# Kernel optimization log

Hardware: AMD Instinct MI355X
Metric: run time of the kernel (lower is better)

The kernel has to match this reference:

```python
import jax, jax.numpy as jnp
import numpy as np

D_MODEL = 1024
N_HEADS = 16
HEAD_DIM = D_MODEL // N_HEADS


def setup_inputs() -> dict:
    key = jax.random.key(0)
    ks = jax.random.split(key, 5)
    x = jax.random.normal(ks[0], (4, 2048, D_MODEL), dtype=jnp.float32)
    # qkv Linear: weight [3*d_model, d_model], bias [3*d_model]
    w_qkv = jax.random.normal(ks[1], (3 * D_MODEL, D_MODEL), dtype=jnp.float32) / np.sqrt(D_MODEL)
    b_qkv = jnp.zeros((3 * D_MODEL,), dtype=jnp.float32)
    w_out = jax.random.normal(ks[2], (D_MODEL, D_MODEL), dtype=jnp.float32) / np.sqrt(D_MODEL)
    b_out = jnp.zeros((D_MODEL,), dtype=jnp.float32)
    return {"x": x, "w_qkv": w_qkv, "b_qkv": b_qkv, "w_out": w_out, "b_out": b_out}


def reference(x, w_qkv, b_qkv, w_out, b_out):
    B, T, C = x.shape
    H, Dh = N_HEADS, HEAD_DIM
    qkv = x @ w_qkv.T + b_qkv                      # [B,T,3C]
    qkv = qkv.reshape(B, T, 3, H, Dh)
    q = jnp.transpose(qkv[:, :, 0], (0, 2, 1, 3))  # [B,H,T,Dh]
    k = jnp.transpose(qkv[:, :, 1], (0, 2, 1, 3))
    v = jnpp_transpose = jnp.transpose(qkv[:, :, 2], (0, 2, 1, 3))
    scale = 1.0 / np.sqrt(Dh).astype(np.float32)
    att = jnp.einsum('bhqd,bhkd->bhqk', q, k) * scale
    causal = jnp.tril(jnp.ones((T, T), dtype=bool))
    att = jnp.where(causal[None, None], att, -jnp.inf)
    att = jax.nn.softmax(att, axis=-1)
    head_out = jnp.einsum('bhqk,bhkd->bhqd', att, v)  # [B,H,T,Dh]
    out = jnp.transpose(head_out, (0, 2, 1, 3)).reshape(B, T, C)
    return out @ w_out.T + b_out
```

## Files before the change

kernel.cpp:

```cpp
#include <hip/hip_runtime.h>
#include <hip/hip_bf16.h>


#define D_MODEL 1024
#define N_HEADS 16
#define HEAD_DIM 64
#define SEQ 2048
#define BATCH 4

typedef __attribute__((ext_vector_type(8))) short bf16x8;
typedef __attribute__((ext_vector_type(4))) float f32x4;
typedef unsigned int uint;

__device__ __forceinline__ short f2bf(float f) {
    union { float f; uint i; } c; c.f = f;
    uint x = c.i;
    x += 0x7fffu + ((x >> 16) & 1u);
    return (short)(x >> 16);
}
__device__ __forceinline__ uint pack2(float a, float b) {
    return (uint)(unsigned short)f2bf(a) | ((uint)(unsigned short)f2bf(b) << 16);
}
__device__ __forceinline__ uint asu(float f) { union { float f; uint i; } c; c.f = f; return c.i; }
__device__ __forceinline__ uint packtr(float lo, float hi) {
    return (asu(lo) >> 16) | (asu(hi) & 0xffff0000u);
}

__device__ __forceinline__ void glds16(const void* g, void* l) {
    __builtin_amdgcn_global_load_lds(
        (const __attribute__((address_space(1))) uint*)g,
        (__attribute__((address_space(3))) uint*)l, 16, 0, 0);
}

__global__ __launch_bounds__(256) void cvt3_bf16(const float* __restrict__ s0,
                                                 const float* __restrict__ s1,
                                                 const float* __restrict__ s2,
                                                 short* __restrict__ dst,
                                                 int n0, int n01) {
    int i = blockIdx.x * 256 + threadIdx.x;
    const float* src;
    int off;
    if (i < n0)       { src = s0; off = i; }
    else if (i < n01) { src = s1; off = i - n0; }
    else              { src = s2; off = i - n01; }
    float4 f = *(const float4*)(src + (size_t)off * 4);
    uint2 o; o.x = pack2(f.x, f.y); o.y = pack2(f.z, f.w);
    *(uint2*)(dst + (size_t)i * 4) = o;
}

template <int MODE>
__global__ __launch_bounds__(256, 2) void gemm_bt(
    const short* __restrict__ A, const short* __restrict__ B,
    const float* __restrict__ bias, float* __restrict__ Cp,
    int M, int N, int K,
    short* __restrict__ qp, short* __restrict__ kp, short* __restrict__ vp)
{
    __shared__ short As[128][32];
    __shared__ short Bs[128][32];
    const int tid = threadIdx.x;
    const int wave = tid >> 6, lane = tid & 63;
    const int quad = lane >> 4, l16 = lane & 15;
    const int wm = (wave >> 1) * 64, wn = (wave & 1) * 64;
    const int rowBase = blockIdx.y * 128;
    const int colBase = blockIdx.x * 128;

    const short* gA = A + (size_t)(rowBase + wave * 32 + (lane >> 2)) * K + (lane & 3) * 8;
    const short* gB = B + (size_t)(colBase + wave * 32 + (lane >> 2)) * K + (lane & 3) * 8;
    void* lA0 = &As[wave * 32][0];
    void* lA1 = &As[wave * 32 + 16][0];
    void* lB0 = &Bs[wave * 32][0];
    void* lB1 = &Bs[wave * 32 + 16][0];

    f32x4 acc[4][4] = {};

    for (int k0 = 0; k0 < K; k0 += 32) {
        __syncthreads();
        glds16(gA + k0, lA0);
        glds16(gA + (size_t)16 * K + k0, lA1);
        glds16(gB + k0, lB0);
        glds16(gB + (size_t)16 * K + k0, lB1);
        __syncthreads();
        bf16x8 af[4], bfr[4];
#pragma unroll
        for (int i = 0; i < 4; ++i)
            af[i] = *(const bf16x8*)&As[wm + i * 16 + l16][quad * 8];
#pragma unroll
        for (int j = 0; j < 4; ++j)
            bfr[j] = *(const bf16x8*)&Bs[wn + j * 16 + l16][quad * 8];
#pragma unroll
        for (int i = 0; i < 4; ++i)
#pragma unroll
            for (int j = 0; j < 4; ++j)
                acc[i][j] = __builtin_amdgcn_mfma_f32_16x16x32_bf16(af[i], bfr[j], acc[i][j], 0, 0, 0);
    }

#pragma unroll
    for (int i = 0; i < 4; ++i) {
#pragma unroll
        for (int j = 0; j < 4; ++j) {
#pragma unroll
            for (int r = 0; r < 4; ++r) {
                int row = rowBase + wm + i * 16 + quad * 4 + r;
                int col = colBase + wn + j * 16 + l16;
                float v = acc[i][j][r] + bias[col];
                if (MODE == 0) {
                    Cp[(size_t)row * N + col] = v;
                } else {
                    int which = col >> 10;
                    int h = (col >> 6) & 15;
                    int d = col & 63;
                    int b = row >> 11;
                    int t = row & 2047;
                    short* dst = (which == 0) ? qp : (which == 1) ? kp : vp;
                    dst[((((size_t)b * N_HEADS + h) * SEQ) + t) * HEAD_DIM + d] = f2bf(v);
                }
            }
        }
    }
}

__global__ __launch_bounds__(256, 2) void attn_fwd(
    const short* __restrict__ Q, const short* __restrict__ K,
    const short* __restrict__ V, short* __restrict__ O)
{
    __shared__ short Ks[64][72];
    __shared__ short Vt[64][72];
    __shared__ short Ps[128][72];
    const int tid = threadIdx.x;
    const int wave = tid >> 6, lane = tid & 63;
    const int quad = lane >> 4, l16 = lane & 15;
    const int bh = blockIdx.x;
    const int b = bh >> 4, h = bh & 15;
    const short* Qh = Q + (size_t)bh * SEQ * HEAD_DIM;
    const short* Kh = K + (size_t)bh * SEQ * HEAD_DIM;
    const short* Vh = V + (size_t)bh * SEQ * HEAD_DIM;

    const float C1 = 0.125f * 1.44269504f;
    const float C2 = 14.4269504f;

    bf16x8 onesf;
#pragma unroll
    for (int e = 0; e < 8; ++e) onesf[e] = (short)0x3F80;

    const int kr = tid >> 2, kc = (tid & 3) * 16;
    const int vk = (tid & 31) * 2, vd = (tid >> 5) * 8;

    for (int pass = 0; pass < 2; ++pass) {
        const int qt = pass == 0 ? (15 - (int)blockIdx.y) : (int)blockIdx.y;
        const int qbase = qt * 128;

        bf16x8 qf[2][2];
#pragma unroll
        for (int m = 0; m < 2; ++m)
#pragma unroll
            for (int st = 0; st < 2; ++st)
                qf[m][st] = *(const bf16x8*)(Qh + (size_t)(qbase + wave * 32 + m * 16 + l16) * HEAD_DIM + st * 32 + quad * 8);

        f32x4 o[2][4] = {};
        f32x4 osum[2] = {};

        const int subw = qbase + wave * 32;
        const int subS = __builtin_amdgcn_readfirstlane(subw);

        const int ntiles = 2 * qt + 2;
        int4 kv0 = *(const int4*)(Kh + (size_t)kr * HEAD_DIM + kc);
        int4 kv1 = *(const int4*)(Kh + (size_t)kr * HEAD_DIM + kc + 8);
        int4 vv0 = *(const int4*)(Vh + (size_t)vk * HEAD_DIM + vd);
        int4 vv1 = *(const int4*)(Vh + (size_t)(vk + 1) * HEAD_DIM + vd);

        for (int j = 0; j < ntiles; ++j) {
            const int kb = j * 64;
            __syncthreads();
            *(int4*)&Ks[kr][kc] = kv0;
            *(int4*)&Ks[kr][kc + 8] = kv1;
            {
                const uint* pa = (const uint*)&vv0;
                const uint* pb = (const uint*)&vv1;
#pragma unroll
                for (int e = 0; e < 4; ++e) {
                    uint lo = __builtin_amdgcn_perm(pb[e], pa[e], 0x05040100u);
                    uint hi = __builtin_amdgcn_perm(pb[e], pa[e], 0x07060302u);
                    *(uint*)&Vt[vd + 2 * e][vk] = lo;
                    *(uint*)&Vt[vd + 2 * e + 1][vk] = hi;
                }
            }
            __syncthreads();

            {
                const int kbn = (j + 1 < ntiles) ? kb + 64 : kb;
                kv0 = *(const int4*)(Kh + (size_t)(kbn + kr) * HEAD_DIM + kc);
                kv1 = *(const int4*)(Kh + (size_t)(kbn + kr) * HEAD_DIM + kc + 8);
                vv0 = *(const int4*)(Vh + (size_t)(kbn + vk) * HEAD_DIM + vd);
                vv1 = *(const int4*)(Vh + (size_t)(kbn + vk + 1) * HEAD_DIM + vd);
            }

            if (kb > subS + 31) continue;

            f32x4 s[2][4];
#pragma unroll
            for (int kt = 0; kt < 4; ++kt) {
                bf16x8 kf0 = *(const bf16x8*)&Ks[kt * 16 + l16][quad * 8];
                bf16x8 kf1 = *(const bf16x8*)&Ks[kt * 16 + l16][32 + quad * 8];
#pragma unroll
                for (int m = 0; m < 2; ++m) {
                    f32x4 t = {0.f, 0.f, 0.f, 0.f};
                    t = __builtin_amdgcn_mfma_f32_16x16x32_bf16(kf0, qf[m][0], t, 0, 0, 0);
                    t = __builtin_amdgcn_mfma_f32_16x16x32_bf16(kf1, qf[m][1], t, 0, 0, 0);
                    s[m][kt] = t;
                }
            }
#pragma unroll
            for (int m = 0; m < 2; ++m) {
                const int sub = subS + m * 16;
                const int qrow = sub + l16;
                const int prow = wave * 32 + m * 16 + l16;
#pragma unroll
                for (int kt = 0; kt < 4; ++kt) {
                    const int kbkt = kb + kt * 16;
                    uint2 u;
                    if (kbkt > sub + 15) {
                        u.x = 0u; u.y = 0u;
                    } else if (kbkt + 15 <= sub) {
                        float p[4];
#pragma unroll
                        for (int r = 0; r < 4; ++r)
                            p[r] = __builtin_exp2f(__builtin_fmaf(s[m][kt][r], C1, -C2));
                        u.x = packtr(p[0], p[1]); u.y = packtr(p[2], p[3]);
                    } else {
                        float p[4];
#pragma unroll
                        for (int r = 0; r < 4; ++r) {
                            float a = __builtin_fmaf(s[m][kt][r], C1, -C2);
                            if (kbkt + quad * 4 + r > qrow) a = -1e30f;
                            p[r] = __builtin_exp2f(a);
                        }
                        u.x = packtr(p[0], p[1]); u.y = packtr(p[2], p[3]);
                    }
                    *(uint2*)&Ps[prow][kt * 16 + quad * 4] = u;
                }
            }
#pragma unroll
            for (int st = 0; st < 2; ++st) {
                bf16x8 pf0 = *(const bf16x8*)&Ps[wave * 32 + l16][st * 32 + quad * 8];
                bf16x8 pf1 = *(const bf16x8*)&Ps[wave * 32 + 16 + l16][st * 32 + quad * 8];
                osum[0] = __builtin_amdgcn_mfma_f32_16x16x32_bf16(pf0, onesf, osum[0], 0, 0, 0);
                osum[1] = __builtin_amdgcn_mfma_f32_16x16x32_bf16(pf1, onesf, osum[1], 0, 0, 0);
#pragma unroll
                for (int dt = 0; dt < 4; ++dt) {
                    bf16x8 vf = *(const bf16x8*)&Vt[dt * 16 + l16][st * 32 + quad * 8];
                    o[0][dt] = __builtin_amdgcn_mfma_f32_16x16x32_bf16(pf0, vf, o[0][dt], 0, 0, 0);
                    o[1][dt] = __builtin_amdgcn_mfma_f32_16x16x32_bf16(pf1, vf, o[1][dt], 0, 0, 0);
                }
            }
        }

#pragma unroll
        for (int m = 0; m < 2; ++m) {
#pragma unroll
            for (int r = 0; r < 4; ++r) {
                float inv = 1.f / osum[m][r];
                int t = qbase + wave * 32 + m * 16 + quad * 4 + r;
                size_t base = ((size_t)b * SEQ + t) * D_MODEL + h * HEAD_DIM;
#pragma unroll
                for (int dt = 0; dt < 4; ++dt)
                    O[base + dt * 16 + l16] = f2bf(o[m][dt][r] * inv);
            }
        }
    }
}

extern "C" void kernel_launch(void* const* d_in, const int* in_sizes, int n_in,
                              void* d_out, int out_size, void* d_ws, size_t ws_size,
                              hipStream_t stream)
{
    const float* x     = (const float*)d_in[0];
    const float* w_qkv = (const float*)d_in[1];
    const float* b_qkv = (const float*)d_in[2];
    const float* w_out = (const float*)d_in[3];
    const float* b_out = (const float*)d_in[4];
    float* out = (float*)d_out;

    const int NX = BATCH * SEQ * D_MODEL;
    const int NWQ = 3 * D_MODEL * D_MODEL;
    const int NWO = D_MODEL * D_MODEL;
    const size_t HE = (size_t)BATCH * N_HEADS * SEQ * HEAD_DIM;

    short* xb    = (short*)d_ws;
    short* wqkvb = xb + NX;
    short* woutb = wqkvb + NWQ;
    short* qp    = woutb + NWO;
    short* kp    = qp + HE;
    short* vp    = kp + HE;
    short* ho    = xb;

    const int M = BATCH * SEQ;

    cvt3_bf16<<<(NX + NWQ + NWO) / 1024, 256, 0, stream>>>(
        x, w_qkv, w_out, xb, NX / 4, (NX + NWQ) / 4);

    gemm_bt<1><<<dim3(3 * D_MODEL / 128, M / 128), 256, 0, stream>>>(
        xb, wqkvb, b_qkv, nullptr, M, 3 * D_MODEL, D_MODEL, qp, kp, vp);

    attn_fwd<<<dim3(BATCH * N_HEADS, SEQ / 256), 256, 0, stream>>>(qp, kp, vp, ho);

    gemm_bt<0><<<dim3(D_MODEL / 128, M / 128), 256, 0, stream>>>(
        ho, woutb, b_out, out, M, D_MODEL, D_MODEL, nullptr, nullptr, nullptr);
}
```

Before: 265.3 us.

## Restructure attention to 512-thread blocks with one query tile each

The attention kernel now launches one 128-row query tile per block with 8 waves of 16 rows each, replacing 4 waves of 32 rows that processed two paired tiles. Half the threads stage V (with transpose) and the other half stage K, and the block order is reversed so the longest causal tiles are scheduled first. The PV step is skipped for the fully masked half of the diagonal tile, and the bf16 truncation pack uses a single byte-permute instruction. The aim is more waves and parallelism per CU and less per-wave register load. The trade-off is that the balanced two-pass pairing is lost, per-CU load balance now relies on the launch order, and more waves share each barrier.

```diff
diff --git a/kernel.cpp b/kernel.cpp
--- a/kernel.cpp
+++ b/kernel.cpp
@@ -23,7 +23,7 @@
 }
 __device__ __forceinline__ uint asu(float f) { union { float f; uint i; } c; c.f = f; return c.i; }
 __device__ __forceinline__ uint packtr(float lo, float hi) {
-    return (asu(lo) >> 16) | (asu(hi) & 0xffff0000u);
+    return __builtin_amdgcn_perm(asu(hi), asu(lo), 0x07060302u);
 }
 
 __device__ __forceinline__ void glds16(const void* g, void* l) {
@@ -119,7 +119,7 @@
     }
 }
 
-__global__ __launch_bounds__(256, 2) void attn_fwd(
+__global__ __launch_bounds__(512, 8) void attn_fwd(
     const short* __restrict__ Q, const short* __restrict__ K,
     const short* __restrict__ V, short* __restrict__ O)
 {
@@ -127,10 +127,12 @@
     __shared__ short Vt[64][72];
     __shared__ short Ps[128][72];
     const int tid = threadIdx.x;
-    const int wave = tid >> 6, lane = tid & 63;
+    const int wq = tid >> 6, lane = tid & 63;
     const int quad = lane >> 4, l16 = lane & 15;
     const int bh = blockIdx.x;
     const int b = bh >> 4, h = bh & 15;
+    const int qt = gridDim.y - 1 - blockIdx.y;
+    const int qbase = qt * 128;
     const short* Qh = Q + (size_t)bh * SEQ * HEAD_DIM;
     const short* Kh = K + (size_t)bh * SEQ * HEAD_DIM;
     const short* Vh = V + (size_t)bh * SEQ * HEAD_DIM;
@@ -142,130 +144,123 @@
 #pragma unroll
     for (int e = 0; e < 8; ++e) onesf[e] = (short)0x3F80;
 
-    const int kr = tid >> 2, kc = (tid & 3) * 16;
-    const int vk = (tid & 31) * 2, vd = (tid >> 5) * 8;
-
-    for (int pass = 0; pass < 2; ++pass) {
-        const int qt = pass == 0 ? (15 - (int)blockIdx.y) : (int)blockIdx.y;
-        const int qbase = qt * 128;
-
-        bf16x8 qf[2][2];
-#pragma unroll
-        for (int m = 0; m < 2; ++m)
-#pragma unroll
-            for (int st = 0; st < 2; ++st)
-                qf[m][st] = *(const bf16x8*)(Qh + (size_t)(qbase + wave * 32 + m * 16 + l16) * HEAD_DIM + st * 32 + quad * 8);
-
-        f32x4 o[2][4] = {};
-        f32x4 osum[2] = {};
-
-        const int subw = qbase + wave * 32;
-        const int subS = __builtin_amdgcn_readfirstlane(subw);
-
-        const int ntiles = 2 * qt + 2;
-        int4 kv0 = *(const int4*)(Kh + (size_t)kr * HEAD_DIM + kc);
-        int4 kv1 = *(const int4*)(Kh + (size_t)kr * HEAD_DIM + kc + 8);
-        int4 vv0 = *(const int4*)(Vh + (size_t)vk * HEAD_DIM + vd);
-        int4 vv1 = *(const int4*)(Vh + (size_t)(vk + 1) * HEAD_DIM + vd);
-
-        for (int j = 0; j < ntiles; ++j) {
-            const int kb = j * 64;
-            __syncthreads();
-            *(int4*)&Ks[kr][kc] = kv0;
-            *(int4*)&Ks[kr][kc + 8] = kv1;
-            {
-                const uint* pa = (const uint*)&vv0;
-                const uint* pb = (const uint*)&vv1;
-#pragma unroll
-                for (int e = 0; e < 4; ++e) {
-                    uint lo = __builtin_amdgcn_perm(pb[e], pa[e], 0x05040100u);
-                    uint hi = __builtin_amdgcn_perm(pb[e], pa[e], 0x07060302u);
-                    *(uint*)&Vt[vd + 2 * e][vk] = lo;
-                    *(uint*)&Vt[vd + 2 * e + 1][vk] = hi;
+    bf16x8 qf[2];
+#pragma unroll
+    for (int st = 0; st < 2; ++st)
+        qf[st] = *(const bf16x8*)(Qh + (size_t)(qbase + wq * 16 + l16) * HEAD_DIM + st * 32 + quad * 8);
+
+    f32x4 o[4] = {};
+    f32x4 osum = {};
+
+    const int subw = qbase + wq * 16;
+    const int subS = __builtin_amdgcn_readfirstlane(subw);
+    const int qrow = subS + l16;
+
+    const int t = tid & 255;
+    const bool vrole = tid < 256;
+    const int kr = t >> 2, kc = (t & 3) * 16;
+    const int vk = (t & 31) * 2, vd = (t >> 5) * 8;
+
+    const int ntiles = 2 * qt + 2;
+    int4 pre0, pre1;
+    if (vrole) {
+        pre0 = *(const int4*)(Vh + (size_t)vk * HEAD_DIM + vd);
+        pre1 = *(const int4*)(Vh + (size_t)(vk + 1) * HEAD_DIM + vd);
+    } else {
+        pre0 = *(const int4*)(Kh + (size_t)kr * HEAD_DIM + kc);
+        pre1 = *(const int4*)(Kh + (size_t)kr * HEAD_DIM + kc + 8);
+    }
+
+    for (int j = 0; j < ntiles; ++j) {
+        const int kb = j * 64;
+        __syncthreads();
+        if (vrole) {
+            const uint* pa = (const uint*)&pre0;
+            const uint* pb = (const uint*)&pre1;
+#pragma unroll
+            for (int e = 0; e < 4; ++e) {
+                uint lo = __builtin_amdgcn_perm(pb[e], pa[e], 0x05040100u);
+                uint hi = __builtin_amdgcn_perm(pb[e], pa[e], 0x07060302u);
+                *(uint*)&Vt[vd + 2 * e][vk] = lo;
+                *(uint*)&Vt[vd + 2 * e + 1][vk] = hi;
+            }
+        } else {
+            *(int4*)&Ks[kr][kc] = pre0;
+            *(int4*)&Ks[kr][kc + 8] = pre1;
+        }
+        __syncthreads();
+
+        {
+            const int kbn = (j + 1 < ntiles) ? kb + 64 : kb;
+            if (vrole) {
+                pre0 = *(const int4*)(Vh + (size_t)(kbn + vk) * HEAD_DIM + vd);
+                pre1 = *(const int4*)(Vh + (size_t)(kbn + vk + 1) * HEAD_DIM + vd);
+            } else {
+                pre0 = *(const int4*)(Kh + (size_t)(kbn + kr) * HEAD_DIM + kc);
+                pre1 = *(const int4*)(Kh + (size_t)(kbn + kr) * HEAD_DIM + kc + 8);
+            }
+        }
+
+        if (kb > subS + 15) continue;
+
+        f32x4 s[4];
+#pragma unroll
+        for (int kt = 0; kt < 4; ++kt) {
+            bf16x8 kf0 = *(const bf16x8*)&Ks[kt * 16 + l16][quad * 8];
+            bf16x8 kf1 = *(const bf16x8*)&Ks[kt * 16 + l16][32 + quad * 8];
+            f32x4 tt = {0.f, 0.f, 0.f, 0.f};
+            tt = __builtin_amdgcn_mfma_f32_16x16x32_bf16(kf0, qf[0], tt, 0, 0, 0);
+            tt = __builtin_amdgcn_mfma_f32_16x16x32_bf16(kf1, qf[1], tt, 0, 0, 0);
+            s[kt] = tt;
+        }
+        {
+            const int prow = wq * 16 + l16;
+#pragma unroll
+            for (int kt = 0; kt < 4; ++kt) {
+                const int kbkt = kb + kt * 16;
+                uint2 u;
+                if (kbkt > subS + 15) {
+                    u.x = 0u; u.y = 0u;
+                } else if (kbkt + 15 <= subS) {
+                    float p[4];
+#pragma unroll
+                    for (int r = 0; r < 4; ++r)
+                        p[r] = __builtin_exp2f(__builtin_fmaf(s[kt][r], C1, -C2));
+                    u.x = packtr(p[0], p[1]); u.y = packtr(p[2], p[3]);
+                } else {
+                    float p[4];
+#pragma unroll
+                    for (int r = 0; r < 4; ++r) {
+                        float a = __builtin_fmaf(s[kt][r], C1, -C2);
+                        if (kbkt + quad * 4 + r > qrow) a = -1e30f;
+                        p[r] = __builtin_exp2f(a);
+                    }
+                    u.x = packtr(p[0], p[1]); u.y = packtr(p[2], p[3]);
                 }
-            }
-            __syncthreads();
-
-            {
-                const int kbn = (j + 1 < ntiles) ? kb + 64 : kb;
-                kv0 = *(const int4*)(Kh + (size_t)(kbn + kr) * HEAD_DIM + kc);
-                kv1 = *(const int4*)(Kh + (size_t)(kbn + kr) * HEAD_DIM + kc + 8);
-                vv0 = *(const int4*)(Vh + (size_t)(kbn + vk) * HEAD_DIM + vd);
-                vv1 = *(const int4*)(Vh + (size_t)(kbn + vk + 1) * HEAD_DIM + vd);
-            }
-
-            if (kb > subS + 31) continue;
-
-            f32x4 s[2][4];
-#pragma unroll
-            for (int kt = 0; kt < 4; ++kt) {
-                bf16x8 kf0 = *(const bf16x8*)&Ks[kt * 16 + l16][quad * 8];
-                bf16x8 kf1 = *(const bf16x8*)&Ks[kt * 16 + l16][32 + quad * 8];
-#pragma unroll
-                for (int m = 0; m < 2; ++m) {
-                    f32x4 t = {0.f, 0.f, 0.f, 0.f};
-                    t = __builtin_amdgcn_mfma_f32_16x16x32_bf16(kf0, qf[m][0], t, 0, 0, 0);
-                    t = __builtin_amdgcn_mfma_f32_16x16x32_bf16(kf1, qf[m][1], t, 0, 0, 0);
-                    s[m][kt] = t;
-                }
-            }
-#pragma unroll
-            for (int m = 0; m < 2; ++m) {
-                const int sub = subS + m * 16;
-                const int qrow = sub + l16;
-                const int prow = wave * 32 + m * 16 + l16;
-#pragma unroll
-                for (int kt = 0; kt < 4; ++kt) {
-                    const int kbkt = kb + kt * 16;
-                    uint2 u;
-                    if (kbkt > sub + 15) {
-                        u.x = 0u; u.y = 0u;
-                    } else if (kbkt + 15 <= sub) {
-                        float p[4];
-#pragma unroll
-                        for (int r = 0; r < 4; ++r)
-                            p[r] = __builtin_exp2f(__builtin_fmaf(s[m][kt][r], C1, -C2));
-                        u.x = packtr(p[0], p[1]); u.y = packtr(p[2], p[3]);
-                    } else {
-                        float p[4];
-#pragma unroll
-                        for (int r = 0; r < 4; ++r) {
-                            float a = __builtin_fmaf(s[m][kt][r], C1, -C2);
-                            if (kbkt + quad * 4 + r > qrow) a = -1e30f;
-                            p[r] = __builtin_exp2f(a);
-                        }
-                        u.x = packtr(p[0], p[1]); u.y = packtr(p[2], p[3]);
-                    }
-                    *(uint2*)&Ps[prow][kt * 16 + quad * 4] = u;
-                }
-            }
-#pragma unroll
-            for (int st = 0; st < 2; ++st) {
-                bf16x8 pf0 = *(const bf16x8*)&Ps[wave * 32 + l16][st * 32 + quad * 8];
-                bf16x8 pf1 = *(const bf16x8*)&Ps[wave * 32 + 16 + l16][st * 32 + quad * 8];
-                osum[0] = __builtin_amdgcn_mfma_f32_16x16x32_bf16(pf0, onesf, osum[0], 0, 0, 0);
-                osum[1] = __builtin_amdgcn_mfma_f32_16x16x32_bf16(pf1, onesf, osum[1], 0, 0, 0);
-#pragma unroll
-                for (int dt = 0; dt < 4; ++dt) {
-                    bf16x8 vf = *(const bf16x8*)&Vt[dt * 16 + l16][st * 32 + quad * 8];
-                    o[0][dt] = __builtin_amdgcn_mfma_f32_16x16x32_bf16(pf0, vf, o[0][dt], 0, 0, 0);
-                    o[1][dt] = __builtin_amdgcn_mfma_f32_16x16x32_bf16(pf1, vf, o[1][dt], 0, 0, 0);
-                }
-            }
-        }
-
-#pragma unroll
-        for (int m = 0; m < 2; ++m) {
-#pragma unroll
-            for (int r = 0; r < 4; ++r) {
-                float inv = 1.f / osum[m][r];
-                int t = qbase + wave * 32 + m * 16 + quad * 4 + r;
-                size_t base = ((size_t)b * SEQ + t) * D_MODEL + h * HEAD_DIM;
-#pragma unroll
-                for (int dt = 0; dt < 4; ++dt)
-                    O[base + dt * 16 + l16] = f2bf(o[m][dt][r] * inv);
-            }
-        }
+                *(uint2*)&Ps[prow][kt * 16 + quad * 4] = u;
+            }
+        }
+#pragma unroll
+        for (int st = 0; st < 2; ++st) {
+            if (st == 1 && kb + 32 > subS + 15) break;
+            bf16x8 pf = *(const bf16x8*)&Ps[wq * 16 + l16][st * 32 + quad * 8];
+            osum = __builtin_amdgcn_mfma_f32_16x16x32_bf16(pf, onesf, osum, 0, 0, 0);
+#pragma unroll
+            for (int dt = 0; dt < 4; ++dt) {
+                bf16x8 vf = *(const bf16x8*)&Vt[dt * 16 + l16][st * 32 + quad * 8];
+                o[dt] = __builtin_amdgcn_mfma_f32_16x16x32_bf16(pf, vf, o[dt], 0, 0, 0);
+            }
+        }
+    }
+
+#pragma unroll
+    for (int r = 0; r < 4; ++r) {
+        float inv = 1.f / osum[r];
+        int trow = qbase + wq * 16 + quad * 4 + r;
+        size_t base = ((size_t)b * SEQ + trow) * D_MODEL + h * HEAD_DIM;
+#pragma unroll
+        for (int dt = 0; dt < 4; ++dt)
+            O[base + dt * 16 + l16] = f2bf(o[dt][r] * inv);
     }
 }
 
@@ -301,7 +296,7 @@
     gemm_bt<1><<<dim3(3 * D_MODEL / 128, M / 128), 256, 0, stream>>>(
         xb, wqkvb, b_qkv, nullptr, M, 3 * D_MODEL, D_MODEL, qp, kp, vp);
 
-    attn_fwd<<<dim3(BATCH * N_HEADS, SEQ / 256), 256, 0, stream>>>(qp, kp, vp, ho);
+    attn_fwd<<<dim3(BATCH * N_HEADS, SEQ / 128), 512, 0, stream>>>(qp, kp, vp, ho);
 
     gemm_bt<0><<<dim3(D_MODEL / 128, M / 128), 256, 0, stream>>>(
         ho, woutb, b_out, out, M, D_MODEL, D_MODEL, nullptr, nullptr, nullptr);
```

Result: slower. 391.1 us (+47.4%).

## One query tile per block, skip masked QK MFMAs, use perm for bf16 packing

Applied to the files above, without the earlier changes.

The attention kernel drops its two-pass paired query-tile scheme. It now launches one block per 128-row query tile, with twice the grid in y and the heaviest tiles scheduled first. QK^T MFMAs and K fragment loads are skipped for 16-key subtiles lying fully above the causal diagonal, and the second PV half-step is skipped when it is fully masked. The bf16 truncation packing now uses a single v_perm. This trades the load balance of pairing light and heavy tiles for more blocks, and relies on the hardware scheduler to balance the uneven per-block work.

```diff
diff --git a/kernel.cpp b/kernel.cpp
--- a/kernel.cpp
+++ b/kernel.cpp
@@ -23,7 +23,7 @@
 }
 __device__ __forceinline__ uint asu(float f) { union { float f; uint i; } c; c.f = f; return c.i; }
 __device__ __forceinline__ uint packtr(float lo, float hi) {
-    return (asu(lo) >> 16) | (asu(hi) & 0xffff0000u);
+    return __builtin_amdgcn_perm(asu(hi), asu(lo), 0x07060302u);
 }
 
 __device__ __forceinline__ void glds16(const void* g, void* l) {
@@ -131,6 +131,8 @@
     const int quad = lane >> 4, l16 = lane & 15;
     const int bh = blockIdx.x;
     const int b = bh >> 4, h = bh & 15;
+    const int qt = gridDim.y - 1 - blockIdx.y;
+    const int qbase = qt * 128;
     const short* Qh = Q + (size_t)bh * SEQ * HEAD_DIM;
     const short* Kh = K + (size_t)bh * SEQ * HEAD_DIM;
     const short* Vh = V + (size_t)bh * SEQ * HEAD_DIM;
@@ -142,129 +144,122 @@
 #pragma unroll
     for (int e = 0; e < 8; ++e) onesf[e] = (short)0x3F80;
 
+    bf16x8 qf[2][2];
+#pragma unroll
+    for (int m = 0; m < 2; ++m)
+#pragma unroll
+        for (int st = 0; st < 2; ++st)
+            qf[m][st] = *(const bf16x8*)(Qh + (size_t)(qbase + wave * 32 + m * 16 + l16) * HEAD_DIM + st * 32 + quad * 8);
+
+    f32x4 o[2][4] = {};
+    f32x4 osum[2] = {};
+
+    const int subw = qbase + wave * 32;
+    const int subS = __builtin_amdgcn_readfirstlane(subw);
+
     const int kr = tid >> 2, kc = (tid & 3) * 16;
     const int vk = (tid & 31) * 2, vd = (tid >> 5) * 8;
 
-    for (int pass = 0; pass < 2; ++pass) {
-        const int qt = pass == 0 ? (15 - (int)blockIdx.y) : (int)blockIdx.y;
-        const int qbase = qt * 128;
-
-        bf16x8 qf[2][2];
-#pragma unroll
-        for (int m = 0; m < 2; ++m)
-#pragma unroll
-            for (int st = 0; st < 2; ++st)
-                qf[m][st] = *(const bf16x8*)(Qh + (size_t)(qbase + wave * 32 + m * 16 + l16) * HEAD_DIM + st * 32 + quad * 8);
-
-        f32x4 o[2][4] = {};
-        f32x4 osum[2] = {};
-
-        const int subw = qbase + wave * 32;
-        const int subS = __builtin_amdgcn_readfirstlane(subw);
-
-        const int ntiles = 2 * qt + 2;
-        int4 kv0 = *(const int4*)(Kh + (size_t)kr * HEAD_DIM + kc);
-        int4 kv1 = *(const int4*)(Kh + (size_t)kr * HEAD_DIM + kc + 8);
-        int4 vv0 = *(const int4*)(Vh + (size_t)vk * HEAD_DIM + vd);
-        int4 vv1 = *(const int4*)(Vh + (size_t)(vk + 1) * HEAD_DIM + vd);
-
-        for (int j = 0; j < ntiles; ++j) {
-            const int kb = j * 64;
-            __syncthreads();
-            *(int4*)&Ks[kr][kc] = kv0;
-            *(int4*)&Ks[kr][kc + 8] = kv1;
-            {
-                const uint* pa = (const uint*)&vv0;
-                const uint* pb = (const uint*)&vv1;
-#pragma unroll
-                for (int e = 0; e < 4; ++e) {
-                    uint lo = __builtin_amdgcn_perm(pb[e], pa[e], 0x05040100u);
-                    uint hi = __builtin_amdgcn_perm(pb[e], pa[e], 0x07060302u);
-                    *(uint*)&Vt[vd + 2 * e][vk] = lo;
-                    *(uint*)&Vt[vd + 2 * e + 1][vk] = hi;
+    const int ntiles = 2 * qt + 2;
+    int4 kv0 = *(const int4*)(Kh + (size_t)kr * HEAD_DIM + kc);
+    int4 kv1 = *(const int4*)(Kh + (size_t)kr * HEAD_DIM + kc + 8);
+    int4 vv0 = *(const int4*)(Vh + (size_t)vk * HEAD_DIM + vd);
+    int4 vv1 = *(const int4*)(Vh + (size_t)(vk + 1) * HEAD_DIM + vd);
+
+    for (int j = 0; j < ntiles; ++j) {
+        const int kb = j * 64;
+        __syncthreads();
+        *(int4*)&Ks[kr][kc] = kv0;
+        *(int4*)&Ks[kr][kc + 8] = kv1;
+        {
+            const uint* pa = (const uint*)&vv0;
+            const uint* pb = (const uint*)&vv1;
+#pragma unroll
+            for (int e = 0; e < 4; ++e) {
+                uint lo = __builtin_amdgcn_perm(pb[e], pa[e], 0x05040100u);
+                uint hi = __builtin_amdgcn_perm(pb[e], pa[e], 0x07060302u);
+                *(uint*)&Vt[vd + 2 * e][vk] = lo;
+                *(uint*)&Vt[vd + 2 * e + 1][vk] = hi;
+            }
+        }
+        __syncthreads();
+
+        {
+            const int kbn = (j + 1 < ntiles) ? kb + 64 : kb;
+            kv0 = *(const int4*)(Kh + (size_t)(kbn + kr) * HEAD_DIM + kc);
+            kv1 = *(const int4*)(Kh + (size_t)(kbn + kr) * HEAD_DIM + kc + 8);
+            vv0 = *(const int4*)(Vh + (size_t)(kbn + vk) * HEAD_DIM + vd);
+            vv1 = *(const int4*)(Vh + (size_t)(kbn + vk + 1) * HEAD_DIM + vd);
+        }
+
+        if (kb > subS + 31) continue;
+
+        {
+            const int prowb = wave * 32 + l16;
+#pragma unroll
+            for (int kt = 0; kt < 4; ++kt) {
+                const int kbkt = kb + kt * 16;
+                bf16x8 kf0, kf1;
+                if (kbkt <= subS + 31) {
+                    kf0 = *(const bf16x8*)&Ks[kt * 16 + l16][quad * 8];
+                    kf1 = *(const bf16x8*)&Ks[kt * 16 + l16][32 + quad * 8];
                 }
-            }
-            __syncthreads();
-
-            {
-                const int kbn = (j + 1 < ntiles) ? kb + 64 : kb;
-                kv0 = *(const int4*)(Kh + (size_t)(kbn + kr) * HEAD_DIM + kc);
-                kv1 = *(const int4*)(Kh + (size_t)(kbn + kr) * HEAD_DIM + kc + 8);
-                vv0 = *(const int4*)(Vh + (size_t)(kbn + vk) * HEAD_DIM + vd);
-                vv1 = *(const int4*)(Vh + (size_t)(kbn + vk + 1) * HEAD_DIM + vd);
-            }
-
-            if (kb > subS + 31) continue;
-
-            f32x4 s[2][4];
-#pragma unroll
-            for (int kt = 0; kt < 4; ++kt) {
-                bf16x8 kf0 = *(const bf16x8*)&Ks[kt * 16 + l16][quad * 8];
-                bf16x8 kf1 = *(const bf16x8*)&Ks[kt * 16 + l16][32 + quad * 8];
 #pragma unroll
                 for (int m = 0; m < 2; ++m) {
-                    f32x4 t = {0.f, 0.f, 0.f, 0.f};
-                    t = __builtin_amdgcn_mfma_f32_16x16x32_bf16(kf0, qf[m][0], t, 0, 0, 0);
-                    t = __builtin_amdgcn_mfma_f32_16x16x32_bf16(kf1, qf[m][1], t, 0, 0, 0);
-                    s[m][kt] = t;
-                }
-            }
-#pragma unroll
-            for (int m = 0; m < 2; ++m) {
-                const int sub = subS + m * 16;
-                const int qrow = sub + l16;
-                const int prow = wave * 32 + m * 16 + l16;
-#pragma unroll
-                for (int kt = 0; kt < 4; ++kt) {
-                    const int kbkt = kb + kt * 16;
+                    const int sub = subS + m * 16;
                     uint2 u;
                     if (kbkt > sub + 15) {
                         u.x = 0u; u.y = 0u;
-                    } else if (kbkt + 15 <= sub) {
+                    } else {
+                        f32x4 tt = {0.f, 0.f, 0.f, 0.f};
+                        tt = __builtin_amdgcn_mfma_f32_16x16x32_bf16(kf0, qf[m][0], tt, 0, 0, 0);
+                        tt = __builtin_amdgcn_mfma_f32_16x16x32_bf16(kf1, qf[m][1], tt, 0, 0, 0);
                         float p[4];
-#pragma unroll
-                        for (int r = 0; r < 4; ++r)
-                            p[r] = __builtin_exp2f(__builtin_fmaf(s[m][kt][r], C1, -C2));
-                        u.x = packtr(p[0], p[1]); u.y = packtr(p[2], p[3]);
-                    } else {
-                        float p[4];
-#pragma unroll
-                        for (int r = 0; r < 4; ++r) {
-                            float a = __builtin_fmaf(s[m][kt][r], C1, -C2);
-                            if (kbkt + quad * 4 + r > qrow) a = -1e30f;
-                            p[r] = __builtin_exp2f(a);
+                        if (kbkt + 15 <= sub) {
+#pragma unroll
+                            for (int r = 0; r < 4; ++r)
+                                p[r] = __builtin_exp2f(__builtin_fmaf(tt[r], C1, -C2));
+                        } else {
+                            const int qrow = sub + l16;
+#pragma unroll
+                            for (int r = 0; r < 4; ++r) {
+                                float a = __builtin_fmaf(tt[r], C1, -C2);
+                                if (kbkt + quad * 4 + r > qrow) a = -1e30f;
+                                p[r] = __builtin_exp2f(a);
+                            }
                         }
                         u.x = packtr(p[0], p[1]); u.y = packtr(p[2], p[3]);
                     }
-                    *(uint2*)&Ps[prow][kt * 16 + quad * 4] = u;
+                    *(uint2*)&Ps[prowb + m * 16][kt * 16 + quad * 4] = u;
                 }
             }
-#pragma unroll
-            for (int st = 0; st < 2; ++st) {
-                bf16x8 pf0 = *(const bf16x8*)&Ps[wave * 32 + l16][st * 32 + quad * 8];
-                bf16x8 pf1 = *(const bf16x8*)&Ps[wave * 32 + 16 + l16][st * 32 + quad * 8];
-                osum[0] = __builtin_amdgcn_mfma_f32_16x16x32_bf16(pf0, onesf, osum[0], 0, 0, 0);
-                osum[1] = __builtin_amdgcn_mfma_f32_16x16x32_bf16(pf1, onesf, osum[1], 0, 0, 0);
-#pragma unroll
-                for (int dt = 0; dt < 4; ++dt) {
-                    bf16x8 vf = *(const bf16x8*)&Vt[dt * 16 + l16][st * 32 + quad * 8];
-                    o[0][dt] = __builtin_amdgcn_mfma_f32_16x16x32_bf16(pf0, vf, o[0][dt], 0, 0, 0);
-                    o[1][dt] = __builtin_amdgcn_mfma_f32_16x16x32_bf16(pf1, vf, o[1][dt], 0, 0, 0);
-                }
+        }
+#pragma unroll
+        for (int st = 0; st < 2; ++st) {
+            if (st == 1 && kb + 32 > subS + 31) break;
+            bf16x8 pf0 = *(const bf16x8*)&Ps[wave * 32 + l16][st * 32 + quad * 8];
+            bf16x8 pf1 = *(const bf16x8*)&Ps[wave * 32 + 16 + l16][st * 32 + quad * 8];
+            osum[0] = __builtin_amdgcn_mfma_f32_16x16x32_bf16(pf0, onesf, osum[0], 0, 0, 0);
+            osum[1] = __builtin_amdgcn_mfma_f32_16x16x32_bf16(pf1, onesf, osum[1], 0, 0, 0);
+#pragma unroll
+            for (int dt = 0; dt < 4; ++dt) {
+                bf16x8 vf = *(const bf16x8*)&Vt[dt * 16 + l16][st * 32 + quad * 8];
+                o[0][dt] = __builtin_amdgcn_mfma_f32_16x16x32_bf16(pf0, vf, o[0][dt], 0, 0, 0);
+                o[1][dt] = __builtin_amdgcn_mfma_f32_16x16x32_bf16(pf1, vf, o[1][dt], 0, 0, 0);
             }
         }
-
-#pragma unroll
-        for (int m = 0; m < 2; ++m) {
-#pragma unroll
-            for (int r = 0; r < 4; ++r) {
-                float inv = 1.f / osum[m][r];
-                int t = qbase + wave * 32 + m * 16 + quad * 4 + r;
-                size_t base = ((size_t)b * SEQ + t) * D_MODEL + h * HEAD_DIM;
-#pragma unroll
-                for (int dt = 0; dt < 4; ++dt)
-                    O[base + dt * 16 + l16] = f2bf(o[m][dt][r] * inv);
-            }
+    }
+
+#pragma unroll
+    for (int m = 0; m < 2; ++m) {
+#pragma unroll
+        for (int r = 0; r < 4; ++r) {
+            float inv = 1.f / osum[m][r];
+            int t = qbase + wave * 32 + m * 16 + quad * 4 + r;
+            size_t base = ((size_t)b * SEQ + t) * D_MODEL + h * HEAD_DIM;
+#pragma unroll
+            for (int dt = 0; dt < 4; ++dt)
+                O[base + dt * 16 + l16] = f2bf(o[m][dt][r] * inv);
         }
     }
 }
@@ -301,7 +296,7 @@
     gemm_bt<1><<<dim3(3 * D_MODEL / 128, M / 128), 256, 0, stream>>>(
         xb, wqkvb, b_qkv, nullptr, M, 3 * D_MODEL, D_MODEL, qp, kp, vp);
 
-    attn_fwd<<<dim3(BATCH * N_HEADS, SEQ / 256), 256, 0, stream>>>(qp, kp, vp, ho);
+    attn_fwd<<<dim3(BATCH * N_HEADS, SEQ / 128), 256, 0, stream>>>(qp, kp, vp, ho);
 
     gemm_bt<0><<<dim3(D_MODEL / 128, M / 128), 256, 0, stream>>>(
         ho, woutb, b_out, out, M, D_MODEL, D_MODEL, nullptr, nullptr, nullptr);
```

Result: faster. 253.4 us (-4.5%).
